# Optimization experiments

Hardware: AMD Instinct MI355X
Metric: run time of the kernel (lower is better)

The kernel has to match this reference:

```python
import jax, jax.numpy as jnp
import numpy as np

S, B, H, E, V, L = 64, 32, 1024, 512, 32000, 2


def setup_inputs() -> dict:
    key = jax.random.key(0)
    ks = jax.random.split(key, 12)
    dl = 1.0 / float(np.sqrt(H))
    u = lambda k, shape, a: jax.random.uniform(k, shape, minval=-a, maxval=a, dtype=jnp.float32)
    return {
        "inputs": jax.random.randint(ks[0], (S, B), 0, V),            # token ids [seq, batch]
        "hidden": jnp.zeros((L, B, H), jnp.float32),                  # init_hidden()
        "emb_W": u(ks[1], (V, E), 0.1),                               # embedding, uniform(-0.1,0.1)
        "Wx0": u(ks[2], (H, E), dl), "Wh0": u(ks[3], (H, H), dl), "bh0": u(ks[4], (H,), dl),
        "Wx1": u(ks[5], (H, H), dl), "Wh1": u(ks[6], (H, H), dl), "bh1": u(ks[7], (H,), dl),
        "Wout": u(ks[8], (V, H), 0.1),                                # output Linear, uniform(-0.1,0.1)
        "bout": jnp.zeros((V,), jnp.float32),                         # output bias zeros
    }


def reference(inputs, hidden, emb_W, Wx0, Wh0, bh0, Wx1, Wh1, bh1, Wout, bout):
    # Embedding lookup for all timesteps (dropout is identity at dp_keep_prob=1.0)
    x = emb_W[inputs]  # [S, B, E]
    Wxs = (Wx0, Wx1)
    Whs = (Wh0, Wh1)
    bs = (bh0, bh1)

    def step(h, x_t):
        # h: [L, B, H]; x_t: [B, E]
        out = x_t
        new_h = []
        for j in range(L):  # fixed small number of structurally distinct layers
            hj = jnp.tanh(out @ Wxs[j].T + h[j] @ Whs[j].T + bs[j])  # vanilla tanh RNN cell
            new_h.append(hj)
            out = hj
        return jnp.stack(new_h), out

    hidden_final, tops = jax.lax.scan(step, hidden, x)  # tops: [S, B, H]
    logits = tops @ Wout.T + bout                        # [S, B, V]
    return logits, hidden_final
```

## Files before the change

### kernel.cpp

```cpp
#include <hip/hip_runtime.h>
#include <hip/hip_bf16.h>

#define S_ 64
#define B_ 32
#define H_ 1024
#define E_ 512
#define V_ 32000

typedef unsigned short ushort_t;
typedef __attribute__((ext_vector_type(8))) short short8;
typedef __attribute__((ext_vector_type(4))) float f32x4;

__device__ __forceinline__ ushort_t f32_bf16(float x) {
    union { float f; unsigned u; } v; v.f = x;
    unsigned r = v.u + 0x7FFF + ((v.u >> 16) & 1);
    return (ushort_t)(r >> 16);
}

__device__ __forceinline__ float bf16_f32(ushort_t x) {
    union { unsigned u; float f; } v; v.u = ((unsigned)x) << 16;
    return v.f;
}


#define WAITV asm volatile("s_waitcnt vmcnt(0)" ::: "memory")
#define SB    __builtin_amdgcn_sched_barrier(0)

__device__ __forceinline__ void ld16n(short8* a, const ushort_t* p) {
    asm volatile(
        "global_load_dwordx4 %0, %16, off offset:0 sc0 sc1\n\t"
        "global_load_dwordx4 %1, %16, off offset:64 sc0 sc1\n\t"
        "global_load_dwordx4 %2, %16, off offset:128 sc0 sc1\n\t"
        "global_load_dwordx4 %3, %16, off offset:192 sc0 sc1\n\t"
        "global_load_dwordx4 %4, %16, off offset:256 sc0 sc1\n\t"
        "global_load_dwordx4 %5, %16, off offset:320 sc0 sc1\n\t"
        "global_load_dwordx4 %6, %16, off offset:384 sc0 sc1\n\t"
        "global_load_dwordx4 %7, %16, off offset:448 sc0 sc1\n\t"
        "global_load_dwordx4 %8, %16, off offset:512 sc0 sc1\n\t"
        "global_load_dwordx4 %9, %16, off offset:576 sc0 sc1\n\t"
        "global_load_dwordx4 %10, %16, off offset:640 sc0 sc1\n\t"
        "global_load_dwordx4 %11, %16, off offset:704 sc0 sc1\n\t"
        "global_load_dwordx4 %12, %16, off offset:768 sc0 sc1\n\t"
        "global_load_dwordx4 %13, %16, off offset:832 sc0 sc1\n\t"
        "global_load_dwordx4 %14, %16, off offset:896 sc0 sc1\n\t"
        "global_load_dwordx4 %15, %16, off offset:960 sc0 sc1"
        : "=&v"(a[0]), "=&v"(a[1]), "=&v"(a[2]), "=&v"(a[3]),
          "=&v"(a[4]), "=&v"(a[5]), "=&v"(a[6]), "=&v"(a[7]),
          "=&v"(a[8]), "=&v"(a[9]), "=&v"(a[10]), "=&v"(a[11]),
          "=&v"(a[12]), "=&v"(a[13]), "=&v"(a[14]), "=&v"(a[15])
        : "v"(p));
}

__device__ __forceinline__ void st2_coh(ushort_t* p, unsigned v) {
    asm volatile("global_store_short %0, %1, off sc0 sc1" :: "v"(p), "v"(v) : "memory");
}

__device__ __forceinline__ void wait_ge(unsigned* c, int tgt) {
    if (tgt <= 0) return;
    if ((threadIdx.x & 63) == 0) {
        int guard = 0;
        while ((int)__hip_atomic_load(c, __ATOMIC_RELAXED, __HIP_MEMORY_SCOPE_AGENT) < tgt &&
               ++guard < (1 << 24))
            __builtin_amdgcn_s_sleep(2);
    }
    __builtin_amdgcn_sched_barrier(0);
}

__device__ __forceinline__ void arrive(unsigned* c) {
    asm volatile("s_waitcnt vmcnt(0)" ::: "memory");
    if ((threadIdx.x & 63) == 0)
        (void)__hip_atomic_fetch_add(c, 1u, __ATOMIC_RELAXED, __HIP_MEMORY_SCOPE_AGENT);
    __builtin_amdgcn_sched_barrier(0);
}

__global__ void cvt_bf16(const float* __restrict__ src, ushort_t* __restrict__ dst, int n4) {
    int i = blockIdx.x * blockDim.x + threadIdx.x;
    int stride = gridDim.x * blockDim.x;
    const float4* s4 = (const float4*)src;
    ushort4* d4 = (ushort4*)dst;
    for (; i < n4; i += stride) {
        float4 v = s4[i];
        ushort4 o;
        o.x = f32_bf16(v.x); o.y = f32_bf16(v.y);
        o.z = f32_bf16(v.z); o.w = f32_bf16(v.w);
        d4[i] = o;
    }
}

__global__ void init_hidden(const float* __restrict__ hid,
                            ushort_t* __restrict__ h0buf, ushort_t* __restrict__ h1buf,
                            unsigned* __restrict__ ctrs) {
    int i = blockIdx.x * blockDim.x + threadIdx.x;
    int j = i & (B_ * H_ - 1);
    if (i < B_ * H_) h0buf[B_ * H_ + j] = f32_bf16(hid[i]);
    else             h1buf[B_ * H_ + j] = f32_bf16(hid[i]);
    if (blockIdx.x == 0 && threadIdx.x < 64) ctrs[threadIdx.x] = 0;
}

__global__ void gather_emb(const int* __restrict__ tok, const float* __restrict__ emb,
                           ushort_t* __restrict__ xb) {
    int m = blockIdx.x;
    int t = tok[m];
    const float4* src = (const float4*)(emb + (long)t * E_);
    ushort4* dst = (ushort4*)(xb + (long)m * E_);
    int i = threadIdx.x;
    float4 v = src[i];
    ushort4 o;
    o.x = f32_bf16(v.x); o.y = f32_bf16(v.y);
    o.z = f32_bf16(v.z); o.w = f32_bf16(v.w);
    dst[i] = o;
}

__global__ __launch_bounds__(256) void xproj_kernel(const ushort_t* __restrict__ Xb,
                                                    const ushort_t* __restrict__ Wx0b,
                                                    const float* __restrict__ bh0,
                                                    float* __restrict__ xproj) {
    int wid = (blockIdx.x * 256 + threadIdx.x) >> 6;
    int lane = threadIdx.x & 63;
    int quad = lane >> 4;
    int nt = wid & 63, mt = wid >> 6;
    int mrow = mt * 16 + (lane & 15);
    int nrow = nt * 16 + (lane & 15);
    const short8* Ap = (const short8*)(Xb + (long)mrow * E_ + quad * 8);
    const short8* Bp = (const short8*)(Wx0b + (long)nrow * E_ + quad * 8);
    f32x4 acc = {0.f, 0.f, 0.f, 0.f};
#pragma unroll
    for (int k = 0; k < E_ / 32; ++k)
        acc = __builtin_amdgcn_mfma_f32_16x16x32_bf16(Ap[k * 4], Bp[k * 4], acc, 0, 0, 0);
    float bias = bh0[nrow];
#pragma unroll
    for (int r = 0; r < 4; ++r) {
        int m = mt * 16 + quad * 4 + r;
        xproj[(long)m * H_ + nrow] = acc[r] + bias;
    }
}

__global__ __launch_bounds__(256, 1) void rnn_steps2(
        const ushort_t* __restrict__ Wh0b,
        const ushort_t* __restrict__ Wx1b,
        const ushort_t* __restrict__ Wh1b,
        const float* __restrict__ bh1,
        const float* __restrict__ xproj,
        ushort_t* __restrict__ h0buf,
        ushort_t* __restrict__ h1buf,
        ushort_t* __restrict__ tops,
        unsigned* __restrict__ ctrs) {
    const int lb = blockIdx.x;
    const int lane = threadIdx.x & 63;
    const int widx = threadIdx.x >> 6;
    const int quad = lane >> 4;
    const int l15 = lane & 15;
    const int wid = (lb & 31) * 4 + widx;
    const int nt = wid & 63, mt = wid >> 6;
    const int b0 = mt * 16 + l15;
    const int h = nt * 16 + l15;
    unsigned* l0c = ctrs;
    unsigned* l1c = ctrs + 32;
    constexpr int BH = B_ * H_;

    if (lb < 32) {
        short8 wf[32];
        const short8* Wr = (const short8*)(Wh0b + (long)h * H_ + quad * 8);
#pragma unroll
        for (int k = 0; k < 32; ++k) wf[k] = Wr[k * 4];
        for (int p = 0; p < S_; ++p) {
            wait_ge(l0c, 128 * p);
            const float* xp = xproj + (long)p * BH;
            float xv[4];
#pragma unroll
            for (int r = 0; r < 4; ++r) xv[r] = xp[(long)(mt * 16 + quad * 4 + r) * H_ + h];
            const ushort_t* Ap = h0buf + ((p + 1) & 1) * BH + (long)b0 * H_ + quad * 8;
            short8 a[32];
            ld16n(a, Ap);
            ld16n(a + 16, Ap + 512);
            WAITV; SB;
            f32x4 aA = {0.f, 0.f, 0.f, 0.f}, aB = {0.f, 0.f, 0.f, 0.f};
#pragma unroll
            for (int k = 0; k < 32; k += 2) {
                aA = __builtin_amdgcn_mfma_f32_16x16x32_bf16(a[k], wf[k], aA, 0, 0, 0);
                aB = __builtin_amdgcn_mfma_f32_16x16x32_bf16(a[k + 1], wf[k + 1], aB, 0, 0, 0);
            }
            float vv[4];
#pragma unroll
            for (int r = 0; r < 4; ++r) vv[r] = tanhf(aA[r] + aB[r] + xv[r]);
            wait_ge(l1c, 128 * (p - 1));
            ushort_t* outp = h0buf + (p & 1) * BH;
#pragma unroll
            for (int r = 0; r < 4; ++r)
                st2_coh(outp + (long)(mt * 16 + quad * 4 + r) * H_ + h, (unsigned)f32_bf16(vv[r]));
            arrive(l0c);
        }
    } else {
        short8 wfx[32], wfh[32];
        const short8* Wxr = (const short8*)(Wx1b + (long)h * H_ + quad * 8);
        const short8* Whr = (const short8*)(Wh1b + (long)h * H_ + quad * 8);
#pragma unroll
        for (int k = 0; k < 32; ++k) { wfx[k] = Wxr[k * 4]; wfh[k] = Whr[k * 4]; }
        const float bias1 = bh1[h];
        for (int p = 1; p <= S_; ++p) {
            const int t = p - 1;
            wait_ge(l0c, 128 * p);
            wait_ge(l1c, 128 * (p - 1));
            const ushort_t* A0 = h0buf + (t & 1) * BH + (long)b0 * H_ + quad * 8;
            const ushort_t* A1 = h1buf + ((t + 1) & 1) * BH + (long)b0 * H_ + quad * 8;
            f32x4 aA = {0.f, 0.f, 0.f, 0.f}, aB = {0.f, 0.f, 0.f, 0.f};
            {
                short8 a0[16], a1[16];
                ld16n(a0, A0); ld16n(a1, A1);
                WAITV; SB;
#pragma unroll
                for (int k = 0; k < 16; ++k) {
                    aA = __builtin_amdgcn_mfma_f32_16x16x32_bf16(a0[k], wfx[k], aA, 0, 0, 0);
                    aB = __builtin_amdgcn_mfma_f32_16x16x32_bf16(a1[k], wfh[k], aB, 0, 0, 0);
                }
            }
            {
                short8 a0[16], a1[16];
                ld16n(a0, A0 + 512); ld16n(a1, A1 + 512);
                WAITV; SB;
#pragma unroll
                for (int k = 0; k < 16; ++k) {
                    aA = __builtin_amdgcn_mfma_f32_16x16x32_bf16(a0[k], wfx[16 + k], aA, 0, 0, 0);
                    aB = __builtin_amdgcn_mfma_f32_16x16x32_bf16(a1[k], wfh[16 + k], aB, 0, 0, 0);
                }
            }
            ushort_t* outp = h1buf + (t & 1) * BH;
            ushort_t* top = tops + (long)t * BH;
#pragma unroll
            for (int r = 0; r < 4; ++r) {
                float v = tanhf(aA[r] + aB[r] + bias1);
                ushort_t bv = f32_bf16(v);
                st2_coh(outp + (long)(mt * 16 + quad * 4 + r) * H_ + h, (unsigned)bv);
                top[(long)(mt * 16 + quad * 4 + r) * H_ + h] = bv;
            }
            arrive(l1c);
        }
    }
}

#define BM 128
#define BN 128
#define BK 32

__device__ __forceinline__ void ld_lds16(const ushort_t* g, ushort_t* l) {
    __builtin_amdgcn_global_load_lds((const __attribute__((address_space(1))) void*)g,
                                     (__attribute__((address_space(3))) void*)l, 16, 0, 0);
}

__global__ __launch_bounds__(256) void out_gemm(const ushort_t* __restrict__ A,
                                                const ushort_t* __restrict__ Bw,
                                                const float* __restrict__ bout,
                                                float* __restrict__ C) {
    __shared__ __align__(16) ushort_t lA[BM * BK];
    __shared__ __align__(16) ushort_t lB[BN * BK];
    int mblk = blockIdx.x;
    int nblk = blockIdx.y;
    int tid = threadIdx.x;
    int lane = tid & 63;
    int w = tid >> 6;
    int quad = lane >> 4;
    int srow = tid >> 2;
    int sslot = (tid & 3) ^ ((srow >> 1) & 3);
    int skol = sslot * 8;
    const ushort_t* Ag = A + (long)(mblk * BM + srow) * H_ + skol;
    const ushort_t* Bg = Bw + (long)(nblk * BN + srow) * H_ + skol;
    ushort_t* lA0 = lA + tid * 8;
    ushort_t* lA1 = lA + 2048 + tid * 8;
    ushort_t* lB0 = lB + tid * 8;
    ushort_t* lB1 = lB + 2048 + tid * 8;

    int msub = (w & 1) * 64;
    int nsub = (w >> 1) * 64;
    int l15 = lane & 15;
    int rquad = quad ^ ((l15 >> 1) & 3);
    f32x4 acc[4][4];
#pragma unroll
    for (int i = 0; i < 4; ++i)
#pragma unroll
        for (int j = 0; j < 4; ++j) acc[i][j] = (f32x4){0.f, 0.f, 0.f, 0.f};

    for (int k0 = 0; k0 < H_; k0 += BK) {
        ld_lds16(Ag + k0, lA0);
        ld_lds16(Ag + 64 * H_ + k0, lA1);
        ld_lds16(Bg + k0, lB0);
        ld_lds16(Bg + 64 * H_ + k0, lB1);
        __syncthreads();
        short8 af[4], bf[4];
#pragma unroll
        for (int i = 0; i < 4; ++i)
            af[i] = *(const short8*)&lA[(msub + i * 16 + l15) * BK + rquad * 8];
#pragma unroll
        for (int j = 0; j < 4; ++j)
            bf[j] = *(const short8*)&lB[(nsub + j * 16 + l15) * BK + rquad * 8];
#pragma unroll
        for (int i = 0; i < 4; ++i)
#pragma unroll
            for (int j = 0; j < 4; ++j)
                acc[i][j] = __builtin_amdgcn_mfma_f32_16x16x32_bf16(af[i], bf[j], acc[i][j], 0, 0, 0);
        __syncthreads();
    }

#pragma unroll
    for (int j = 0; j < 4; ++j) {
        int n = nblk * BN + nsub + j * 16 + l15;
        float bo = bout[n];
#pragma unroll
        for (int i = 0; i < 4; ++i) {
#pragma unroll
            for (int r = 0; r < 4; ++r) {
                int m = mblk * BM + msub + i * 16 + quad * 4 + r;
                C[(long)m * V_ + n] = acc[i][j][r] + bo;
            }
        }
    }
}

__global__ void final_hidden(const ushort_t* __restrict__ h0buf,
                             const ushort_t* __restrict__ h1buf,
                             float* __restrict__ out) {
    int i = blockIdx.x * blockDim.x + threadIdx.x;
    int j = i & (B_ * H_ - 1);
    ushort_t v = (i < B_ * H_) ? h0buf[B_ * H_ + j] : h1buf[B_ * H_ + j];
    out[(long)S_ * B_ * V_ + i] = bf16_f32(v);
}

extern "C" void kernel_launch(void* const* d_in, const int* in_sizes, int n_in,
                              void* d_out, int out_size, void* d_ws, size_t ws_size,
                              hipStream_t stream) {
    const int*   tok  = (const int*)d_in[0];
    const float* hid  = (const float*)d_in[1];
    const float* emb  = (const float*)d_in[2];
    const float* Wx0  = (const float*)d_in[3];
    const float* Wh0  = (const float*)d_in[4];
    const float* bh0  = (const float*)d_in[5];
    const float* Wx1  = (const float*)d_in[6];
    const float* Wh1  = (const float*)d_in[7];
    const float* bh1  = (const float*)d_in[8];
    const float* Wout = (const float*)d_in[9];
    const float* bout = (const float*)d_in[10];
    float* out = (float*)d_out;

    char* ws = (char*)d_ws;
    size_t off = 0;
    ushort_t* woutb = (ushort_t*)(ws + off); off += (size_t)V_ * H_ * 2;
    ushort_t* wh0b  = (ushort_t*)(ws + off); off += (size_t)H_ * H_ * 2;
    ushort_t* wx1b  = (ushort_t*)(ws + off); off += (size_t)H_ * H_ * 2;
    ushort_t* wh1b  = (ushort_t*)(ws + off); off += (size_t)H_ * H_ * 2;
    ushort_t* wx0b  = (ushort_t*)(ws + off); off += (size_t)H_ * E_ * 2;
    ushort_t* xb    = (ushort_t*)(ws + off); off += (size_t)S_ * B_ * E_ * 2;
    float*    xproj = (float*)(ws + off);    off += (size_t)S_ * B_ * H_ * 4;
    ushort_t* topsb = (ushort_t*)(ws + off); off += (size_t)S_ * B_ * H_ * 2;
    ushort_t* h0b   = (ushort_t*)(ws + off); off += (size_t)2 * B_ * H_ * 2;
    ushort_t* h1b   = (ushort_t*)(ws + off); off += (size_t)2 * B_ * H_ * 2;
    unsigned* ctrs  = (unsigned*)(ws + off); off += 256;

    cvt_bf16<<<2048, 256, 0, stream>>>(Wout, woutb, V_ * H_ / 4);
    cvt_bf16<<<256, 256, 0, stream>>>(Wh0, wh0b, H_ * H_ / 4);
    cvt_bf16<<<256, 256, 0, stream>>>(Wx1, wx1b, H_ * H_ / 4);
    cvt_bf16<<<256, 256, 0, stream>>>(Wh1, wh1b, H_ * H_ / 4);
    cvt_bf16<<<128, 256, 0, stream>>>(Wx0, wx0b, H_ * E_ / 4);
    init_hidden<<<256, 256, 0, stream>>>(hid, h0b, h1b, ctrs);
    gather_emb<<<S_ * B_, 128, 0, stream>>>(tok, emb, xb);
    xproj_kernel<<<2048, 256, 0, stream>>>(xb, wx0b, bh0, xproj);
    rnn_steps2<<<64, 256, 0, stream>>>(wh0b, wx1b, wh1b, bh1, xproj, h0b, h1b, topsb, ctrs);
    out_gemm<<<dim3(16, 250), 256, 0, stream>>>(topsb, woutb, bout, out);
    final_hidden<<<256, 256, 0, stream>>>(h0b, h1b, out);
}
```

Baseline: 1.569 ms.

## Replace atomic counters with per-wave flags polled by whole wavefront

After: 1.424 ms. -9.2%, faster.

```diff
diff --git a/kernel.cpp b/kernel.cpp
--- a/kernel.cpp
+++ b/kernel.cpp
@@ -55,21 +55,30 @@
     asm volatile("global_store_short %0, %1, off sc0 sc1" :: "v"(p), "v"(v) : "memory");
 }
 
-__device__ __forceinline__ void wait_ge(unsigned* c, int tgt) {
-    if (tgt <= 0) return;
-    if ((threadIdx.x & 63) == 0) {
-        int guard = 0;
-        while ((int)__hip_atomic_load(c, __ATOMIC_RELAXED, __HIP_MEMORY_SCOPE_AGENT) < tgt &&
-               ++guard < (1 << 24))
-            __builtin_amdgcn_s_sleep(2);
+__device__ __forceinline__ void wait2(const unsigned* flags, int tA, int tB) {
+    if (tA <= 0 && tB <= 0) return;
+    const int lane = threadIdx.x & 63;
+    const unsigned* p = flags + lane * 4;
+    const int tgt = (lane < 32) ? tA : tB;
+    for (int it = 0; it < (1 << 22); ++it) {
+        uint4 v;
+        asm volatile("global_load_dwordx4 %0, %1, off sc0 sc1\n\t"
+                     "s_waitcnt vmcnt(0)"
+                     : "=v"(v) : "v"(p) : "memory");
+        int m = (int)v.x;
+        m = m < (int)v.y ? m : (int)v.y;
+        m = m < (int)v.z ? m : (int)v.z;
+        m = m < (int)v.w ? m : (int)v.w;
+        if (__all(m >= tgt)) break;
+        __builtin_amdgcn_s_sleep(1);
     }
     __builtin_amdgcn_sched_barrier(0);
 }
 
-__device__ __forceinline__ void arrive(unsigned* c) {
+__device__ __forceinline__ void set_flag(unsigned* fl, unsigned val) {
     asm volatile("s_waitcnt vmcnt(0)" ::: "memory");
     if ((threadIdx.x & 63) == 0)
-        (void)__hip_atomic_fetch_add(c, 1u, __ATOMIC_RELAXED, __HIP_MEMORY_SCOPE_AGENT);
+        asm volatile("global_store_dword %0, %1, off sc0 sc1" :: "v"(fl), "v"(val) : "memory");
     __builtin_amdgcn_sched_barrier(0);
 }
 
@@ -89,12 +98,12 @@
 
 __global__ void init_hidden(const float* __restrict__ hid,
                             ushort_t* __restrict__ h0buf, ushort_t* __restrict__ h1buf,
-                            unsigned* __restrict__ ctrs) {
+                            unsigned* __restrict__ flags) {
     int i = blockIdx.x * blockDim.x + threadIdx.x;
     int j = i & (B_ * H_ - 1);
     if (i < B_ * H_) h0buf[B_ * H_ + j] = f32_bf16(hid[i]);
     else             h1buf[B_ * H_ + j] = f32_bf16(hid[i]);
-    if (blockIdx.x == 0 && threadIdx.x < 64) ctrs[threadIdx.x] = 0;
+    if (blockIdx.x == 0 && threadIdx.x < 256) flags[threadIdx.x] = 0;
 }
 
 __global__ void gather_emb(const int* __restrict__ tok, const float* __restrict__ emb,
@@ -144,7 +153,7 @@
         ushort_t* __restrict__ h0buf,
         ushort_t* __restrict__ h1buf,
         ushort_t* __restrict__ tops,
-        unsigned* __restrict__ ctrs) {
+        unsigned* __restrict__ flags) {
     const int lb = blockIdx.x;
     const int lane = threadIdx.x & 63;
     const int widx = threadIdx.x >> 6;
@@ -154,21 +163,20 @@
     const int nt = wid & 63, mt = wid >> 6;
     const int b0 = mt * 16 + l15;
     const int h = nt * 16 + l15;
-    unsigned* l0c = ctrs;
-    unsigned* l1c = ctrs + 32;
     constexpr int BH = B_ * H_;
 
     if (lb < 32) {
+        unsigned* myflag = flags + wid;
         short8 wf[32];
         const short8* Wr = (const short8*)(Wh0b + (long)h * H_ + quad * 8);
 #pragma unroll
         for (int k = 0; k < 32; ++k) wf[k] = Wr[k * 4];
         for (int p = 0; p < S_; ++p) {
-            wait_ge(l0c, 128 * p);
             const float* xp = xproj + (long)p * BH;
             float xv[4];
 #pragma unroll
             for (int r = 0; r < 4; ++r) xv[r] = xp[(long)(mt * 16 + quad * 4 + r) * H_ + h];
+            wait2(flags, p, 0);
             const ushort_t* Ap = h0buf + ((p + 1) & 1) * BH + (long)b0 * H_ + quad * 8;
             short8 a[32];
             ld16n(a, Ap);
@@ -183,24 +191,23 @@
             float vv[4];
 #pragma unroll
             for (int r = 0; r < 4; ++r) vv[r] = tanhf(aA[r] + aB[r] + xv[r]);
-            wait_ge(l1c, 128 * (p - 1));
+            wait2(flags, 0, p - 1);
             ushort_t* outp = h0buf + (p & 1) * BH;
 #pragma unroll
             for (int r = 0; r < 4; ++r)
                 st2_coh(outp + (long)(mt * 16 + quad * 4 + r) * H_ + h, (unsigned)f32_bf16(vv[r]));
-            arrive(l0c);
+            set_flag(myflag, (unsigned)(p + 1));
         }
     } else {
+        unsigned* myflag = flags + 128 + wid;
         short8 wfx[32], wfh[32];
         const short8* Wxr = (const short8*)(Wx1b + (long)h * H_ + quad * 8);
         const short8* Whr = (const short8*)(Wh1b + (long)h * H_ + quad * 8);
 #pragma unroll
         for (int k = 0; k < 32; ++k) { wfx[k] = Wxr[k * 4]; wfh[k] = Whr[k * 4]; }
         const float bias1 = bh1[h];
-        for (int p = 1; p <= S_; ++p) {
-            const int t = p - 1;
-            wait_ge(l0c, 128 * p);
-            wait_ge(l1c, 128 * (p - 1));
+        for (int t = 0; t < S_; ++t) {
+            wait2(flags, t + 1, t);
             const ushort_t* A0 = h0buf + (t & 1) * BH + (long)b0 * H_ + quad * 8;
             const ushort_t* A1 = h1buf + ((t + 1) & 1) * BH + (long)b0 * H_ + quad * 8;
             f32x4 aA = {0.f, 0.f, 0.f, 0.f}, aB = {0.f, 0.f, 0.f, 0.f};
@@ -233,7 +240,7 @@
                 st2_coh(outp + (long)(mt * 16 + quad * 4 + r) * H_ + h, (unsigned)bv);
                 top[(long)(mt * 16 + quad * 4 + r) * H_ + h] = bv;
             }
-            arrive(l1c);
+            set_flag(myflag, (unsigned)(t + 1));
         }
     }
 }
@@ -352,17 +359,17 @@
     ushort_t* topsb = (ushort_t*)(ws + off); off += (size_t)S_ * B_ * H_ * 2;
     ushort_t* h0b   = (ushort_t*)(ws + off); off += (size_t)2 * B_ * H_ * 2;
     ushort_t* h1b   = (ushort_t*)(ws + off); off += (size_t)2 * B_ * H_ * 2;
-    unsigned* ctrs  = (unsigned*)(ws + off); off += 256;
+    unsigned* flags = (unsigned*)(ws + off); off += 1024;
 
     cvt_bf16<<<2048, 256, 0, stream>>>(Wout, woutb, V_ * H_ / 4);
     cvt_bf16<<<256, 256, 0, stream>>>(Wh0, wh0b, H_ * H_ / 4);
     cvt_bf16<<<256, 256, 0, stream>>>(Wx1, wx1b, H_ * H_ / 4);
     cvt_bf16<<<256, 256, 0, stream>>>(Wh1, wh1b, H_ * H_ / 4);
     cvt_bf16<<<128, 256, 0, stream>>>(Wx0, wx0b, H_ * E_ / 4);
-    init_hidden<<<256, 256, 0, stream>>>(hid, h0b, h1b, ctrs);
+    init_hidden<<<256, 256, 0, stream>>>(hid, h0b, h1b, flags);
     gather_emb<<<S_ * B_, 128, 0, stream>>>(tok, emb, xb);
     xproj_kernel<<<2048, 256, 0, stream>>>(xb, wx0b, bh0, xproj);
-    rnn_steps2<<<64, 256, 0, stream>>>(wh0b, wx1b, wh1b, bh1, xproj, h0b, h1b, topsb, ctrs);
+    rnn_steps2<<<64, 256, 0, stream>>>(wh0b, wx1b, wh1b, bh1, xproj, h0b, h1b, topsb, flags);
     out_gemm<<<dim3(16, 250), 256, 0, stream>>>(topsb, woutb, bout, out);
     final_hidden<<<256, 256, 0, stream>>>(h0b, h1b, out);
 }
```
